# Kernel optimization log

Measured on AMD Instinct MI355X. Metric: run time of the kernel, lower is better.

The kernel has to match this reference:

```python
import jax, jax.numpy as jnp
import numpy as np
from jax import lax

HIDDEN = 50


def setup_inputs() -> dict:
    key = jax.random.key(0)
    ks = jax.random.split(key, 8)
    B, T, I, H, O = 8192, 256, 1, HIDDEN, 1
    s = 0.1  # small init scale, keeps tanh/sigmoid in a sane range
    return {
        "x": jax.random.normal(ks[0], (B, T, I), dtype=jnp.float32),
        "W_ih": jax.random.normal(ks[1], (4 * H, I), dtype=jnp.float32) * s,
        "W_hh": jax.random.normal(ks[2], (4 * H, H), dtype=jnp.float32) * s,
        "b_ih": jax.random.normal(ks[3], (4 * H,), dtype=jnp.float32) * s,
        "b_hh": jax.random.normal(ks[4], (4 * H,), dtype=jnp.float32) * s,
        "W_lin": jax.random.normal(ks[5], (O, H), dtype=jnp.float32) * s,
        "b_lin": jax.random.normal(ks[6], (O,), dtype=jnp.float32) * s,
    }


def reference(x, W_ih, W_hh, b_ih, b_hh, W_lin, b_lin):
    # Single-layer batch_first LSTM; PyTorch gate order is (i, f, g, o).
    # lstm_out[:, -1] == final hidden state h_T for num_layers=1, so we only
    # carry (h, c) and never materialize the full [B, T, H] output.
    # Dropout is identity in eval mode.
    B = x.shape[0]
    b = b_ih + b_hh  # [4H]

    def step(carry, x_t):
        h, c = carry  # [B, H] each
        gates = x_t @ W_ih.T + h @ W_hh.T + b  # [B, 4H]
        i, f, g, o = jnp.split(gates, 4, axis=-1)
        i = jax.nn.sigmoid(i)
        f = jax.nn.sigmoid(f)
        g = jnp.tanh(g)
        o = jax.nn.sigmoid(o)
        c = f * c + i * g
        h = o * jnp.tanh(c)
        return (h, c), None

    xs = jnp.swapaxes(x, 0, 1)  # [T, B, I]
    h0 = jnp.zeros((B, HIDDEN), dtype=x.dtype)
    (hT, _), _ = lax.scan(step, (h0, h0), xs)
    return hT @ W_lin.T + b_lin  # [B, output_size]
```

## Files before the change

### kernel.cpp

```cpp
#include <hip/hip_runtime.h>


#define NTH 832
#define TST 256
#define MB 16
#define NBLK 512
#define HR 72
#define HSZ (MB * HR)

#define LOG2E 1.44269504088896f

typedef __attribute__((ext_vector_type(8))) _Float16 half8;
typedef __attribute__((ext_vector_type(4))) float float4v;

__device__ __forceinline__ float rcp_(float v)  { return __builtin_amdgcn_rcpf(v); }
__device__ __forceinline__ float exp2_(float v) { return __builtin_amdgcn_exp2f(v); }
__device__ __forceinline__ unsigned short f16bits(float v) {
    _Float16 h = (_Float16)v;
    return *(unsigned short*)&h;
}

__global__ __launch_bounds__(NTH, 7) void lstm_mfma(
    const float* __restrict__ x,
    const float* __restrict__ W_ih,
    const float* __restrict__ W_hh,
    const float* __restrict__ b_ih,
    const float* __restrict__ b_hh,
    const float* __restrict__ W_lin,
    const float* __restrict__ b_lin,
    float* __restrict__ out)
{
    __shared__ __align__(16) unsigned short Hh[2 * HSZ];

    const int tid  = threadIdx.x;
    const int wv   = tid >> 6;
    const int ln   = tid & 63;
    const int lrow = ln & 15;
    const int quad = ln >> 4;
    const int bbase = (int)blockIdx.x * MB;
    const int T = wv;

    half8 wh[2], wl[2];
    {
        const int gr = T * 16 + lrow;
        const int j  = gr >> 2, g = gr & 3;
        const int row = g * 50 + j;
        const float scl = (g == 2) ? (2.0f * LOG2E) : (-LOG2E);
        #pragma unroll
        for (int q2 = 0; q2 < 2; ++q2) {
            half8 h8, l8;
            #pragma unroll
            for (int i = 0; i < 8; ++i) {
                const int k = q2 * 32 + quad * 8 + i;
                float V = 0.0f;
                if (j < 50) {
                    if (k < 50)       V = W_hh[row * 50 + k];
                    else if (k == 50) V = W_ih[row];
                    else if (k == 51) V = b_ih[row] + b_hh[row];
                }
                V *= scl;
                _Float16 hi = (_Float16)V;
                h8[i] = hi;
                l8[i] = (_Float16)(V - (float)hi);
            }
            wh[q2] = h8;
            wl[q2] = l8;
        }
    }

    for (int i = tid; i < HSZ; i += NTH)
        ((unsigned int*)Hh)[i] = 0u;
    __syncthreads();
    if (tid < MB) {
        float xv = x[(bbase + tid) * TST + 0];
        Hh[tid * HR + 50] = f16bits(xv);
        Hh[tid * HR + 51] = 0x3C00;
        Hh[HSZ + tid * HR + 51] = 0x3C00;
    }
    __syncthreads();

    float c = 0.0f;
    const float* xb = &x[(bbase + lrow) * TST];
    const unsigned short* Hr = &Hh[lrow * HR + quad * 8];
    unsigned short*       Hw = &Hh[lrow * HR + T * 4 + quad];
    const bool xlane   = (wv == 12) && (quad == 2);
    const bool skiplan = (wv == 12) && (quad == 3);
    const float4v z4 = {0.f, 0.f, 0.f, 0.f};

    auto step1 = [&](int roff, int woff, float xnext) {
        const half8 b0 = *(const half8*)(Hr + roff);
        const half8 b1 = *(const half8*)(Hr + roff + 32);

        float4v a4;
        a4 = __builtin_amdgcn_mfma_f32_16x16x32_f16(wh[0], b0, z4, 0, 0, 0);
        a4 = __builtin_amdgcn_mfma_f32_16x16x32_f16(wh[1], b1, a4, 0, 0, 0);
        a4 = __builtin_amdgcn_mfma_f32_16x16x32_f16(wl[0], b0, a4, 0, 0, 0);
        a4 = __builtin_amdgcn_mfma_f32_16x16x32_f16(wl[1], b1, a4, 0, 0, 0);

        float i_ = rcp_(1.0f + exp2_(a4[0]));
        float f_ = rcp_(1.0f + exp2_(a4[1]));
        float g_ = fmaf(-2.0f, rcp_(exp2_(a4[2]) + 1.0f), 1.0f);
        float o_ = rcp_(1.0f + exp2_(a4[3]));
        float cn = f_ * c + i_ * g_;
        c = cn;
        float th = fmaf(-2.0f, rcp_(exp2_(2.0f * LOG2E * cn) + 1.0f), 1.0f);
        float hn = o_ * th;

        if (xlane) hn = xnext;
        if (!skiplan)
            Hw[woff] = f16bits(hn);
        __syncthreads();
    };

    #pragma unroll 1
    for (int t2 = 0; t2 < TST / 2; ++t2) {
        const int t = t2 * 2;
        float xA = 0.0f, xB = 0.0f;
        if (wv == 12) {
            xA = xb[t + 1];
            xB = xb[(t + 2 < TST) ? (t + 2) : (TST - 1)];
        }
        step1(0,   HSZ, xA);
        step1(HSZ, 0,   xB);
    }

    if (tid < MB) {
        float s = b_lin[0];
        #pragma unroll 10
        for (int k = 0; k < 50; ++k) {
            float hk = (float)(*(const _Float16*)&Hh[tid * HR + k]);
            s += hk * W_lin[k];
        }
        out[bbase + tid] = s;
    }
}

extern "C" void kernel_launch(void* const* d_in, const int* in_sizes, int n_in,
                              void* d_out, int out_size, void* d_ws, size_t ws_size,
                              hipStream_t stream) {
    const float* x     = (const float*)d_in[0];
    const float* W_ih  = (const float*)d_in[1];
    const float* W_hh  = (const float*)d_in[2];
    const float* b_ih  = (const float*)d_in[3];
    const float* b_hh  = (const float*)d_in[4];
    const float* W_lin = (const float*)d_in[5];
    const float* b_lin = (const float*)d_in[6];
    float* out = (float*)d_out;

    lstm_mfma<<<dim3(NBLK), dim3(NTH), 0, stream>>>(
        x, W_ih, W_hh, b_ih, b_hh, W_lin, b_lin, out);
}
```

Baseline: 232.9 us.

## Stage x in LDS and apply input weight and bias in fp32 outside MFMA

Preloads the block's whole x slice into shared memory with vectorized float4 loads. The per-step global x reads by wave 12, and the hidden-state lanes that carried x and a constant 1, are removed. The input projection and bias are now added in fp32 after the MFMAs using per-lane registers, which also makes them more precise. The hi and lo MFMA chains are split into two independent accumulators to shorten the dependency chain. The cost is extra LDS (about 17KB), which may reduce occupancy, plus a few more VALU ops per step.

```diff
diff --git a/kernel.cpp b/kernel.cpp
--- a/kernel.cpp
+++ b/kernel.cpp
@@ -7,6 +7,7 @@
 #define NBLK 512
 #define HR 72
 #define HSZ (MB * HR)
+#define XR 17
 
 #define LOG2E 1.44269504088896f
 
@@ -31,6 +32,7 @@
     float* __restrict__ out)
 {
     __shared__ __align__(16) unsigned short Hh[2 * HSZ];
+    __shared__ __align__(16) float xs[TST * XR];
 
     const int tid  = threadIdx.x;
     const int wv   = tid >> 6;
@@ -39,6 +41,7 @@
     const int quad = ln >> 4;
     const int bbase = (int)blockIdx.x * MB;
     const int T = wv;
+    const int ju = T * 4 + quad;
 
     half8 wh[2], wl[2];
     {
@@ -52,13 +55,7 @@
             #pragma unroll
             for (int i = 0; i < 8; ++i) {
                 const int k = q2 * 32 + quad * 8 + i;
-                float V = 0.0f;
-                if (j < 50) {
-                    if (k < 50)       V = W_hh[row * 50 + k];
-                    else if (k == 50) V = W_ih[row];
-                    else if (k == 51) V = b_ih[row] + b_hh[row];
-                }
-                V *= scl;
+                float V = (j < 50 && k < 50) ? W_hh[row * 50 + k] * scl : 0.0f;
                 _Float16 hi = (_Float16)V;
                 h8[i] = hi;
                 l8[i] = (_Float16)(V - (float)hi);
@@ -68,60 +65,69 @@
         }
     }
 
+    float wihs[4], biass[4];
+    #pragma unroll
+    for (int g = 0; g < 4; ++g) {
+        const float scl = (g == 2) ? (2.0f * LOG2E) : (-LOG2E);
+        if (ju < 50) {
+            wihs[g]  = W_ih[g * 50 + ju] * scl;
+            biass[g] = (b_ih[g * 50 + ju] + b_hh[g * 50 + ju]) * scl;
+        } else {
+            wihs[g] = 0.0f; biass[g] = 0.0f;
+        }
+    }
+
+    for (int idx = tid; idx < MB * TST / 4; idx += NTH) {
+        const int b  = idx >> 6;
+        const int t0 = (idx & 63) * 4;
+        const float4 v4 = *(const float4*)&x[(bbase + b) * TST + t0];
+        xs[(t0 + 0) * XR + b] = v4.x;
+        xs[(t0 + 1) * XR + b] = v4.y;
+        xs[(t0 + 2) * XR + b] = v4.z;
+        xs[(t0 + 3) * XR + b] = v4.w;
+    }
     for (int i = tid; i < HSZ; i += NTH)
         ((unsigned int*)Hh)[i] = 0u;
     __syncthreads();
-    if (tid < MB) {
-        float xv = x[(bbase + tid) * TST + 0];
-        Hh[tid * HR + 50] = f16bits(xv);
-        Hh[tid * HR + 51] = 0x3C00;
-        Hh[HSZ + tid * HR + 51] = 0x3C00;
-    }
-    __syncthreads();
 
     float c = 0.0f;
-    const float* xb = &x[(bbase + lrow) * TST];
     const unsigned short* Hr = &Hh[lrow * HR + quad * 8];
-    unsigned short*       Hw = &Hh[lrow * HR + T * 4 + quad];
-    const bool xlane   = (wv == 12) && (quad == 2);
-    const bool skiplan = (wv == 12) && (quad == 3);
+    unsigned short*       Hw = &Hh[lrow * HR + ju];
+    const float*          Xr = &xs[lrow];
     const float4v z4 = {0.f, 0.f, 0.f, 0.f};
 
-    auto step1 = [&](int roff, int woff, float xnext) {
+    auto step1 = [&](int t, int roff, int woff) {
+        const float xv = Xr[t * XR];
         const half8 b0 = *(const half8*)(Hr + roff);
         const half8 b1 = *(const half8*)(Hr + roff + 32);
 
-        float4v a4;
-        a4 = __builtin_amdgcn_mfma_f32_16x16x32_f16(wh[0], b0, z4, 0, 0, 0);
-        a4 = __builtin_amdgcn_mfma_f32_16x16x32_f16(wh[1], b1, a4, 0, 0, 0);
-        a4 = __builtin_amdgcn_mfma_f32_16x16x32_f16(wl[0], b0, a4, 0, 0, 0);
-        a4 = __builtin_amdgcn_mfma_f32_16x16x32_f16(wl[1], b1, a4, 0, 0, 0);
+        float4v u, v;
+        u = __builtin_amdgcn_mfma_f32_16x16x32_f16(wh[0], b0, z4, 0, 0, 0);
+        v = __builtin_amdgcn_mfma_f32_16x16x32_f16(wl[0], b0, z4, 0, 0, 0);
+        u = __builtin_amdgcn_mfma_f32_16x16x32_f16(wh[1], b1, u, 0, 0, 0);
+        v = __builtin_amdgcn_mfma_f32_16x16x32_f16(wl[1], b1, v, 0, 0, 0);
 
-        float i_ = rcp_(1.0f + exp2_(a4[0]));
-        float f_ = rcp_(1.0f + exp2_(a4[1]));
-        float g_ = fmaf(-2.0f, rcp_(exp2_(a4[2]) + 1.0f), 1.0f);
-        float o_ = rcp_(1.0f + exp2_(a4[3]));
-        float cn = f_ * c + i_ * g_;
+        const float a0 = fmaf(xv, wihs[0], u[0] + v[0]) + biass[0];
+        const float a1 = fmaf(xv, wihs[1], u[1] + v[1]) + biass[1];
+        const float a2 = fmaf(xv, wihs[2], u[2] + v[2]) + biass[2];
+        const float a3 = fmaf(xv, wihs[3], u[3] + v[3]) + biass[3];
+
+        const float i_ = rcp_(1.0f + exp2_(a0));
+        const float f_ = rcp_(1.0f + exp2_(a1));
+        const float g_ = fmaf(-2.0f, rcp_(exp2_(a2) + 1.0f), 1.0f);
+        const float o_ = rcp_(1.0f + exp2_(a3));
+        const float cn = f_ * c + i_ * g_;
         c = cn;
-        float th = fmaf(-2.0f, rcp_(exp2_(2.0f * LOG2E * cn) + 1.0f), 1.0f);
-        float hn = o_ * th;
-
-        if (xlane) hn = xnext;
-        if (!skiplan)
-            Hw[woff] = f16bits(hn);
+        const float th = fmaf(-2.0f, rcp_(exp2_(2.0f * LOG2E * cn) + 1.0f), 1.0f);
+        const float hn = o_ * th;
+        Hw[woff] = f16bits(hn);
         __syncthreads();
     };
 
     #pragma unroll 1
     for (int t2 = 0; t2 < TST / 2; ++t2) {
-        const int t = t2 * 2;
-        float xA = 0.0f, xB = 0.0f;
-        if (wv == 12) {
-            xA = xb[t + 1];
-            xB = xb[(t + 2 < TST) ? (t + 2) : (TST - 1)];
-        }
-        step1(0,   HSZ, xA);
-        step1(HSZ, 0,   xB);
+        step1(2 * t2,     0,   HSZ);
+        step1(2 * t2 + 1, HSZ, 0);
     }
 
     if (tid < MB) {
```

Measured after the change: 286.6 us. +23.0%, slower.
